# Kernel optimization log

Hardware: AMD Instinct MI355X
Metric: run time of the kernel (lower is better)

## Reference

```python
import math
import jax, jax.numpy as jnp
import numpy as np

N_HEADS = 32
ALIBI_BIAS_MAX = 8


def _alibi_slopes(n_heads, alibi_bias_max=8):
    _n = 2 ** math.ceil(math.log2(n_heads))
    m = jnp.arange(1, _n + 1, dtype=jnp.float32) * (alibi_bias_max / _n)
    slopes = 1.0 / jnp.power(2.0, m)
    if _n != n_heads:
        slopes = jnp.concatenate([slopes[1::2], slopes[::2]])[:n_heads]
    return slopes  # [H]


def setup_inputs() -> dict:
    key = jax.random.key(0)
    k1, k2, k3 = jax.random.split(key, 3)
    B, S, D = 1, 2048, 4096
    x = jax.random.normal(k1, (B, S, D), dtype=jnp.float32)
    w_qkv = jax.random.normal(k2, (3 * D, D), dtype=jnp.float32) * 0.02
    b_qkv = jnp.zeros((3 * D,), dtype=jnp.float32)
    w_out = jax.random.normal(k3, (D, D), dtype=jnp.float32) * 0.02
    b_out = jnp.zeros((D,), dtype=jnp.float32)
    return {"x": x, "w_qkv": w_qkv, "b_qkv": b_qkv, "w_out": w_out, "b_out": b_out}


def reference(x, w_qkv, b_qkv, w_out, b_out):
    B, S, D = x.shape
    H = N_HEADS
    hd = D // H
    # fused QKV projection (weights stored [Out, In], out_first=True)
    qkv = jnp.einsum("bsd,od->bso", x, w_qkv) + b_qkv  # [B,S,3D]
    q, k, v = jnp.split(qkv, 3, axis=-1)
    q = q.reshape(B, S, H, hd)
    k = k.reshape(B, S, H, hd)
    v = v.reshape(B, S, H, hd)
    scale = 1.0 / math.sqrt(hd)
    scores = jnp.einsum("bqhd,bkhd->bhqk", q, k) * scale  # [B,H,S,S]
    # ALiBi bias: slopes[h] * arange(1-KSeqLen, 1), broadcast over query pos
    slopes = _alibi_slopes(H, ALIBI_BIAS_MAX)  # [H]
    positions = jnp.arange(1 - S, 1, dtype=jnp.float32)  # [S] key positions
    alibi = slopes[:, None] * positions[None, :]  # [H, S_k]
    scores = scores + alibi[None, :, None, :]
    # causal mask
    causal = jnp.arange(S)[:, None] >= jnp.arange(S)[None, :]  # [Sq, Sk]
    scores = jnp.where(causal[None, None, :, :], scores, jnp.float32(-1e9))
    attn = jax.nn.softmax(scores, axis=-1)
    out = jnp.einsum("bhqk,bkhd->bqhd", attn, v).reshape(B, S, D)
    return jnp.einsum("bsd,od->bso", out, w_out) + b_out
```

## Files before the change

kernel.cpp:

```cpp
#include <hip/hip_runtime.h>
#include <hip/hip_bf16.h>

typedef __bf16 bf16;
typedef __attribute__((ext_vector_type(8))) __bf16 bf16x8;
typedef __attribute__((ext_vector_type(4))) float f32x4;

#define GLOAD_LDS16(g, l)                                                        \
    __builtin_amdgcn_global_load_lds(                                            \
        (const __attribute__((address_space(1))) void*)(g),                      \
        (__attribute__((address_space(3))) void*)(l), 16, 0, 0)

#define WAITV(n) asm volatile("s_waitcnt vmcnt(" #n ")" ::: "memory")
#define BAR()    __builtin_amdgcn_s_barrier()
#define SCHEDB() __builtin_amdgcn_sched_barrier(0)

__global__ __launch_bounds__(256) void cvt_f32_bf16(
    const float* __restrict__ src, bf16* __restrict__ dst, int n16)
{
    int idx = blockIdx.x * 256 + threadIdx.x;
    const int stride = gridDim.x * 256;
    for (int i = idx; i < n16; i += stride) {
        const float* p = src + (size_t)i * 16;
        f32x4 a = *(const f32x4*)p;
        f32x4 b = *(const f32x4*)(p + 4);
        f32x4 c = *(const f32x4*)(p + 8);
        f32x4 d = *(const f32x4*)(p + 12);
        bf16x8 h0, h1;
#pragma unroll
        for (int j = 0; j < 4; ++j) {
            h0[j] = (bf16)a[j]; h0[4 + j] = (bf16)b[j];
            h1[j] = (bf16)c[j]; h1[4 + j] = (bf16)d[j];
        }
        bf16* q = dst + (size_t)i * 16;
        *(bf16x8*)q = h0;
        *(bf16x8*)(q + 8) = h1;
    }
}

template <int OUT_BF16>
__global__ __launch_bounds__(512, 2) void gemm_sp(
    const bf16* __restrict__ A, const bf16* __restrict__ B,
    const float* __restrict__ bias, void* __restrict__ Cout,
    int K, int ldc, int nbx)
{
    constexpr int ASZ = 128 * 64;
    constexpr int BUF = ASZ + 256 * 64;
    __shared__ bf16 lds[3 * BUF];

    int bx, by;
    if ((nbx & 15) == 0) {
        const int r = (int)blockIdx.x & 255;
        const int slot = r >> 3;
        bx = ((int)blockIdx.x >> 8) * 16 + (r & 7) * 2 + (slot >> 4);
        by = slot & 15;
    } else {
        const int cpx = gridDim.x >> 3;
        const int swz = ((int)blockIdx.x & 7) * cpx + ((int)blockIdx.x >> 3);
        bx = swz % nbx; by = swz / nbx;
    }
    const int brow = by * 128, bcol = bx * 256;

    const int tid  = threadIdx.x;
    const int wv   = tid >> 6, lane = tid & 63;
    const int lo   = lane & 15, hi = lane >> 4;
    const int wrp  = wv >> 2, wcp = wv & 3;

    const int srow = lane >> 3;
    const int scol = ((lane & 7) ^ (lane >> 3)) * 8;

    f32x4 acc[4][4];
#pragma unroll
    for (int m = 0; m < 4; ++m)
#pragma unroll
        for (int n = 0; n < 4; ++n)
            acc[m][n] = (f32x4){0.f, 0.f, 0.f, 0.f};

    auto STAGE = [&](int t) {
        const int k0 = t * 64;
        bf16* lb = &lds[(t % 3) * BUF];
#pragma unroll
        for (int j = 0; j < 2; ++j) {
            const int c = wv * 2 + j;
            GLOAD_LDS16(A + (size_t)(brow + c * 8 + srow) * K + k0 + scol, lb + c * 512);
        }
#pragma unroll
        for (int j = 0; j < 4; ++j) {
            const int c = wv * 4 + j;
            GLOAD_LDS16(B + (size_t)(bcol + c * 8 + srow) * K + k0 + scol, lb + ASZ + c * 512);
        }
    };

    const int nt = K / 64;

    STAGE(0); STAGE(1);
    WAITV(6); BAR(); SCHEDB();

    for (int t = 0; t < nt; ++t) {
        const bf16* lb = &lds[(t % 3) * BUF];

        bf16x8 af[4][2], bfr[4][2];
#pragma unroll
        for (int m = 0; m < 4; ++m) {
            const int ru = wrp * 64 + m * 16 + lo;
#pragma unroll
            for (int kk = 0; kk < 2; ++kk)
                af[m][kk] = *(const bf16x8*)&lb[ru * 64 + (((kk * 4 + hi) ^ (lo & 7)) * 8)];
        }
#pragma unroll
        for (int n = 0; n < 4; ++n) {
            const int rb = wcp * 64 + n * 16 + lo;
#pragma unroll
            for (int kk = 0; kk < 2; ++kk)
                bfr[n][kk] = *(const bf16x8*)&lb[ASZ + rb * 64 + (((kk * 4 + hi) ^ (lo & 7)) * 8)];
        }

        if (t + 2 < nt) STAGE(t + 2);

        __builtin_amdgcn_s_setprio(1);
#pragma unroll
        for (int m = 0; m < 4; ++m)
#pragma unroll
            for (int n = 0; n < 4; ++n)
#pragma unroll
                for (int kk = 0; kk < 2; ++kk)
                    acc[m][n] = __builtin_amdgcn_mfma_f32_16x16x32_bf16(af[m][kk], bfr[n][kk], acc[m][n], 0, 0, 0);
        __builtin_amdgcn_s_setprio(0);

        if (t + 2 < nt)      WAITV(6);
        else if (t + 1 < nt) WAITV(0);
        if (t + 1 < nt) { BAR(); SCHEDB(); }
    }

#pragma unroll
    for (int m = 0; m < 4; ++m) {
        const int row = brow + wrp * 64 + m * 16 + hi * 4;
#pragma unroll
        for (int n = 0; n < 4; ++n) {
            const int col = bcol + wcp * 64 + n * 16 + lo;
            const float bv = bias[col];
#pragma unroll
            for (int r = 0; r < 4; ++r) {
                const float v = acc[m][n][r] + bv;
                if (OUT_BF16)
                    ((bf16*)Cout)[(size_t)(row + r) * ldc + col] = (bf16)v;
                else
                    ((float*)Cout)[(size_t)(row + r) * ldc + col] = v;
            }
        }
    }
}

__global__ __launch_bounds__(512) void attn_mfma(
    const bf16* __restrict__ qkv, bf16* __restrict__ attn_out)
{
    const int S = 2048, QKV = 12288, D = 4096, HD = 128;
    const int bid = blockIdx.x;
    const int h   = bid & 31;
    const int qi  = 15 - (bid >> 5);
    const int q0  = qi * 128;
    const int tid = threadIdx.x;
    const int w    = tid >> 6, lane = tid & 63;
    const int lo   = lane & 15, hi = lane >> 4;
    const int qbase = q0 + w * 16;

    __shared__ bf16 Ks[64 * 128];
    __shared__ bf16 Vs[128 * 72];
    __shared__ bf16 Ps[8 * 16 * 72];

    const float scale = 0.08838834764831845f;
    const float slope = exp2f(-0.25f * (float)(h + 1));

    bf16x8 qfrag[4];
#pragma unroll
    for (int ds = 0; ds < 4; ++ds)
        qfrag[ds] = *(const bf16x8*)(qkv + (size_t)(qbase + lo) * QKV + h * HD + ds * 32 + hi * 8);

    f32x4 o[8];
#pragma unroll
    for (int dt = 0; dt < 8; ++dt) o[dt] = (f32x4){0.f, 0.f, 0.f, 0.f};
    float mrow[4] = {-1e30f, -1e30f, -1e30f, -1e30f};
    float lrow[4] = {0.f, 0.f, 0.f, 0.f};

    const int krow = tid >> 3;
    const int kch  = tid & 7;
    const int vp2  = tid & 63;
    const int voct = tid >> 6;

    const int ntile = (q0 + 128) / 64;
    for (int t = 0; t < ntile; ++t) {
        const int kv0 = t * 64;
        {
            const bf16* kp = qkv + (size_t)(kv0 + krow) * QKV + D + h * HD + kch * 16;
            bf16x8 k0 = *(const bf16x8*)kp;
            bf16x8 k1 = *(const bf16x8*)(kp + 8);
            const int kb  = krow * 128 + kch * 16;
            const int swzk = (krow & 7) << 3;
            *(bf16x8*)&Ks[kb ^ swzk]       = k0;
            *(bf16x8*)&Ks[(kb + 8) ^ swzk] = k1;
        }
        {
            const bf16* vp = qkv + (size_t)(kv0 + voct * 8) * QKV + 2 * D + h * HD + 2 * vp2;
            bf16x8 r0, r1;
#pragma unroll
            for (int j = 0; j < 8; ++j) {
                const unsigned u = *(const unsigned*)(vp + (size_t)j * QKV);
                unsigned short us0 = (unsigned short)(u & 0xffff);
                unsigned short us1 = (unsigned short)(u >> 16);
                r0[j] = *(const bf16*)&us0;
                r1[j] = *(const bf16*)&us1;
            }
            *(bf16x8*)&Vs[(2 * vp2) * 72 + voct * 8]     = r0;
            *(bf16x8*)&Vs[(2 * vp2 + 1) * 72 + voct * 8] = r1;
        }
        __syncthreads();

        if (kv0 <= qbase + 15) {
            f32x4 c[4];
#pragma unroll
            for (int j = 0; j < 4; ++j) c[j] = (f32x4){0.f, 0.f, 0.f, 0.f};
            __builtin_amdgcn_s_setprio(1);
#pragma unroll
            for (int ds = 0; ds < 4; ++ds) {
#pragma unroll
                for (int j = 0; j < 4; ++j) {
                    const int r = j * 16 + lo;
                    bf16x8 b = *(const bf16x8*)&Ks[(r * 128 + ds * 32 + hi * 8) ^ ((r & 7) << 3)];
                    c[j] = __builtin_amdgcn_mfma_f32_16x16x32_bf16(qfrag[ds], b, c[j], 0, 0, 0);
                }
            }
            __builtin_amdgcn_s_setprio(0);
#pragma unroll
            for (int r = 0; r < 4; ++r) {
                const int q = qbase + hi * 4 + r;
                float s[4];
#pragma unroll
                for (int j = 0; j < 4; ++j) {
                    const int ki = kv0 + j * 16 + lo;
                    s[j] = c[j][r] * scale + slope * (float)(ki - (S - 1));
                    if (ki > q) s[j] = -1e30f;
                }
                float tm = fmaxf(fmaxf(s[0], s[1]), fmaxf(s[2], s[3]));
                tm = fmaxf(tm, __shfl_xor(tm, 1));
                tm = fmaxf(tm, __shfl_xor(tm, 2));
                tm = fmaxf(tm, __shfl_xor(tm, 4));
                tm = fmaxf(tm, __shfl_xor(tm, 8));
                const float mnew = fmaxf(mrow[r], tm);
                const float cr = __expf(mrow[r] - mnew);
                float p[4], ps = 0.f;
#pragma unroll
                for (int j = 0; j < 4; ++j) { p[j] = __expf(s[j] - mnew); ps += p[j]; }
                ps += __shfl_xor(ps, 1);
                ps += __shfl_xor(ps, 2);
                ps += __shfl_xor(ps, 4);
                ps += __shfl_xor(ps, 8);
                lrow[r] = lrow[r] * cr + ps;
                mrow[r] = mnew;
#pragma unroll
                for (int dt = 0; dt < 8; ++dt) o[dt][r] *= cr;
#pragma unroll
                for (int j = 0; j < 4; ++j)
                    Ps[w * 1152 + (hi * 4 + r) * 72 + j * 16 + lo] = (bf16)p[j];
            }
            bf16x8 pa0 = *(const bf16x8*)&Ps[w * 1152 + lo * 72 + hi * 8];
            bf16x8 pa1 = *(const bf16x8*)&Ps[w * 1152 + lo * 72 + 32 + hi * 8];
            __builtin_amdgcn_s_setprio(1);
#pragma unroll
            for (int dt = 0; dt < 8; ++dt) {
                bf16x8 bv0 = *(const bf16x8*)&Vs[(dt * 16 + lo) * 72 + hi * 8];
                bf16x8 bv1 = *(const bf16x8*)&Vs[(dt * 16 + lo) * 72 + 32 + hi * 8];
                o[dt] = __builtin_amdgcn_mfma_f32_16x16x32_bf16(pa0, bv0, o[dt], 0, 0, 0);
                o[dt] = __builtin_amdgcn_mfma_f32_16x16x32_bf16(pa1, bv1, o[dt], 0, 0, 0);
            }
            __builtin_amdgcn_s_setprio(0);
        }
        __syncthreads();
    }

#pragma unroll
    for (int r = 0; r < 4; ++r) {
        const float inv = 1.0f / lrow[r];
        const int q = qbase + hi * 4 + r;
        bf16* op = attn_out + (size_t)q * D + h * HD;
#pragma unroll
        for (int dt = 0; dt < 8; ++dt)
            op[dt * 16 + lo] = (bf16)(o[dt][r] * inv);
    }
}

extern "C" void kernel_launch(void* const* d_in, const int* in_sizes, int n_in,
                              void* d_out, int out_size, void* d_ws, size_t ws_size,
                              hipStream_t stream) {
    const int S = 2048, D = 4096, QKV = 12288;
    const int NH = 6144;
    const float* x     = (const float*)d_in[0];
    const float* w_qkv = (const float*)d_in[1];
    const float* b_qkv = (const float*)d_in[2];
    const float* w_out = (const float*)d_in[3];
    const float* b_out = (const float*)d_in[4];
    float* out = (float*)d_out;

    char* ws = (char*)d_ws;
    const size_t need_full = (size_t)S * D * 2 + (size_t)QKV * D * 2 + (size_t)S * QKV * 2;

    if (ws_size >= need_full) {
        bf16* xb    = (bf16*)ws;
        bf16* attnb = xb;
        bf16* wqb   = (bf16*)(ws + (size_t)S * D * 2);
        bf16* wob   = wqb;
        bf16* qkvb  = (bf16*)(ws + (size_t)S * D * 2 + (size_t)QKV * D * 2);

        cvt_f32_bf16<<<2048, 256, 0, stream>>>(x, xb, S * D / 16);
        cvt_f32_bf16<<<4096, 256, 0, stream>>>(w_qkv, wqb, QKV * D / 16);
        gemm_sp<1><<<(QKV / 256) * (S / 128), 512, 0, stream>>>(xb, wqb, b_qkv, qkvb, D, QKV, QKV / 256);
        attn_mfma<<<512, 512, 0, stream>>>(qkvb, attnb);
        cvt_f32_bf16<<<2048, 256, 0, stream>>>(w_out, wob, D * D / 16);
        gemm_sp<0><<<(D / 256) * (S / 128), 512, 0, stream>>>(attnb, wob, b_out, out, D, D, D / 256);
    } else {
        bf16* xb    = (bf16*)ws;
        bf16* attnb = xb;
        bf16* wb    = (bf16*)(ws + (size_t)S * D * 2);
        bf16* wob   = wb;
        bf16* qkvb  = (bf16*)(ws + (size_t)S * D * 2 + (size_t)NH * D * 2);

        cvt_f32_bf16<<<2048, 256, 0, stream>>>(x, xb, S * D / 16);
        cvt_f32_bf16<<<2048, 256, 0, stream>>>(w_qkv, wb, NH * D / 16);
        gemm_sp<1><<<(NH / 256) * (S / 128), 512, 0, stream>>>(xb, wb, b_qkv, qkvb, D, QKV, NH / 256);
        cvt_f32_bf16<<<2048, 256, 0, stream>>>(w_qkv + (size_t)NH * D, wb, NH * D / 16);
        gemm_sp<1><<<(NH / 256) * (S / 128), 512, 0, stream>>>(xb, wb, b_qkv + NH, qkvb + NH, D, QKV, NH / 256);
        attn_mfma<<<512, 512, 0, stream>>>(qkvb, attnb);
        cvt_f32_bf16<<<2048, 256, 0, stream>>>(w_out, wob, D * D / 16);
        gemm_sp<0><<<(D / 256) * (S / 128), 512, 0, stream>>>(attnb, wob, b_out, out, D, D, D / 256);
    }
}
```

Baseline: 435.0 us.

## Add 256x256-tile ping-pong GEMM with interleaved staging for QKV projection

Adds a new gemm_8p kernel that computes a 256x256 output tile per 512-thread block (each wave holds 8x4 accumulators) with a double-buffered LDS layout. Each K-step is split into four quarter-MFMA phases, and global->LDS staging for the next step is interleaved between them. Barriers and setprio calls are placed to get ping-pong overlap across waves. The QKV projection now uses this kernel with half as many blocks, which raises arithmetic intensity per block; the cost is more register pressure, many barriers, and fewer blocks in the grid (384) for the occupancy target.

New measurement: 465.6 us. 7.0% more time.

```diff
diff --git a/kernel.cpp b/kernel.cpp
--- a/kernel.cpp
+++ b/kernel.cpp
@@ -11,6 +11,7 @@
         (__attribute__((address_space(3))) void*)(l), 16, 0, 0)
 
 #define WAITV(n) asm volatile("s_waitcnt vmcnt(" #n ")" ::: "memory")
+#define LGKM0()  asm volatile("s_waitcnt lgkmcnt(0)" ::: "memory")
 #define BAR()    __builtin_amdgcn_s_barrier()
 #define SCHEDB() __builtin_amdgcn_sched_barrier(0)
 
@@ -38,6 +39,153 @@
 }
 
 template <int OUT_BF16>
+__global__ __launch_bounds__(512, 2) void gemm_8p(
+    const bf16* __restrict__ A, const bf16* __restrict__ B,
+    const float* __restrict__ bias, void* __restrict__ Cout,
+    int K, int ldc, int nbx)
+{
+    __shared__ bf16 lds[2 * 4 * 8192];
+
+    const int cpx = gridDim.x >> 3;
+    const int swz = ((int)blockIdx.x & 7) * cpx + ((int)blockIdx.x >> 3);
+    const int bx = swz % nbx, by = swz / nbx;
+    const int brow = by * 256, bcol = bx * 256;
+
+    const int tid  = threadIdx.x;
+    const int wv   = tid >> 6, lane = tid & 63;
+    const int lo   = lane & 15, hi = lane >> 4;
+    const int wrp  = wv >> 2, wcp = wv & 3;
+
+    const int srow = lane >> 3;
+    const int scol = ((lane & 7) ^ (lane >> 3)) * 8;
+
+    f32x4 acc[8][4];
+#pragma unroll
+    for (int m = 0; m < 8; ++m)
+#pragma unroll
+        for (int n = 0; n < 4; ++n)
+            acc[m][n] = (f32x4){0.f, 0.f, 0.f, 0.f};
+
+    auto STAGEA = [&](int t, int half) {
+        bf16* lb = &lds[(t & 1) * 32768 + half * 8192];
+        const bf16* gb = A + (size_t)(brow + half * 128) * K + t * 64;
+#pragma unroll
+        for (int j = 0; j < 2; ++j) {
+            const int c = wv * 2 + j;
+            GLOAD_LDS16(gb + (size_t)(c * 8 + srow) * K + scol, lb + c * 512);
+        }
+    };
+    auto STAGEB = [&](int t, int half) {
+        bf16* lb = &lds[(t & 1) * 32768 + (2 + half) * 8192];
+        const bf16* gb = B + (size_t)(bcol + half * 128) * K + t * 64;
+#pragma unroll
+        for (int j = 0; j < 2; ++j) {
+            const int c = wv * 2 + j;
+            GLOAD_LDS16(gb + (size_t)(c * 8 + srow) * K + scol, lb + c * 512);
+        }
+    };
+
+    bf16x8 af[4][2], bf0[2][2], bf1[2][2];
+    auto LDA = [&](int b, int mh) {
+        const bf16* base = &lds[b * 32768 + wrp * 8192];
+#pragma unroll
+        for (int m = 0; m < 4; ++m)
+#pragma unroll
+            for (int kk = 0; kk < 2; ++kk)
+                af[m][kk] = *(const bf16x8*)&base[(mh * 64 + m * 16 + lo) * 64 + (((kk * 4 + hi) ^ (lo & 7)) * 8)];
+    };
+    auto LDB = [&](int b, int nh, bf16x8 (&bfr)[2][2]) {
+        const bf16* base = &lds[b * 32768 + (2 + (wcp >> 1)) * 8192];
+#pragma unroll
+        for (int n = 0; n < 2; ++n)
+#pragma unroll
+            for (int kk = 0; kk < 2; ++kk)
+                bfr[n][kk] = *(const bf16x8*)&base[((wcp & 1) * 64 + nh * 32 + n * 16 + lo) * 64 + (((kk * 4 + hi) ^ (lo & 7)) * 8)];
+    };
+
+#define MM(mh, nh, BF)                                                                     \
+    do {                                                                                   \
+        __builtin_amdgcn_s_setprio(1);                                                     \
+        _Pragma("unroll")                                                                  \
+        for (int m = 0; m < 4; ++m)                                                        \
+            _Pragma("unroll")                                                              \
+            for (int n = 0; n < 2; ++n)                                                    \
+                _Pragma("unroll")                                                          \
+                for (int kk = 0; kk < 2; ++kk)                                             \
+                    acc[(mh) * 4 + m][(nh) * 2 + n] = __builtin_amdgcn_mfma_f32_16x16x32_bf16( \
+                        af[m][kk], BF[n][kk], acc[(mh) * 4 + m][(nh) * 2 + n], 0, 0, 0);   \
+        __builtin_amdgcn_s_setprio(0);                                                     \
+    } while (0)
+
+    const int nt = K / 64, niter = nt / 2;
+
+    STAGEA(0, 0); STAGEA(0, 1); STAGEB(0, 0); STAGEB(0, 1);
+    STAGEA(1, 0); STAGEA(1, 1); STAGEB(1, 0); STAGEB(1, 1);
+    WAITV(8); BAR(); SCHEDB();
+
+    for (int it = 0; it < niter; ++it) {
+        const int t0 = 2 * it;
+        const bool nl = (it + 1 < niter);
+
+        LDA(0, 0); LDB(0, 0, bf0);
+        BAR(); LGKM0(); SCHEDB();
+        MM(0, 0, bf0);
+        BAR();
+        LDB(0, 1, bf1);
+        BAR(); LGKM0(); SCHEDB();
+        MM(0, 1, bf1);
+        BAR();
+        LDA(0, 1);
+        if (nl) { STAGEB(t0 + 2, 0); STAGEB(t0 + 2, 1); }
+        BAR(); LGKM0(); SCHEDB();
+        MM(1, 1, bf1);
+        BAR();
+        if (nl) { STAGEA(t0 + 2, 0); STAGEA(t0 + 2, 1); }
+        BAR(); SCHEDB();
+        MM(1, 0, bf0);
+        if (nl) WAITV(8); else WAITV(0);
+        BAR(); SCHEDB();
+
+        LDA(1, 0); LDB(1, 0, bf0);
+        BAR(); LGKM0(); SCHEDB();
+        MM(0, 0, bf0);
+        BAR();
+        LDB(1, 1, bf1);
+        BAR(); LGKM0(); SCHEDB();
+        MM(0, 1, bf1);
+        BAR();
+        LDA(1, 1);
+        if (nl) { STAGEB(t0 + 3, 0); STAGEB(t0 + 3, 1); }
+        BAR(); LGKM0(); SCHEDB();
+        MM(1, 1, bf1);
+        BAR();
+        if (nl) { STAGEA(t0 + 3, 0); STAGEA(t0 + 3, 1); }
+        BAR(); SCHEDB();
+        MM(1, 0, bf0);
+        if (nl) { WAITV(8); BAR(); SCHEDB(); }
+    }
+#undef MM
+
+#pragma unroll
+    for (int mi = 0; mi < 8; ++mi) {
+        const int row = brow + wrp * 128 + mi * 16 + hi * 4;
+#pragma unroll
+        for (int ni = 0; ni < 4; ++ni) {
+            const int col = bcol + wcp * 64 + ni * 16 + lo;
+            const float bv = bias[col];
+#pragma unroll
+            for (int r = 0; r < 4; ++r) {
+                const float v = acc[mi][ni][r] + bv;
+                if (OUT_BF16)
+                    ((bf16*)Cout)[(size_t)(row + r) * ldc + col] = (bf16)v;
+                else
+                    ((float*)Cout)[(size_t)(row + r) * ldc + col] = v;
+            }
+        }
+    }
+}
+
+template <int OUT_BF16>
 __global__ __launch_bounds__(512, 2) void gemm_sp(
     const bf16* __restrict__ A, const bf16* __restrict__ B,
     const float* __restrict__ bias, void* __restrict__ Cout,
@@ -91,13 +239,11 @@
     };
 
     const int nt = K / 64;
-
     STAGE(0); STAGE(1);
     WAITV(6); BAR(); SCHEDB();
 
     for (int t = 0; t < nt; ++t) {
         const bf16* lb = &lds[(t % 3) * BUF];
-
         bf16x8 af[4][2], bfr[4][2];
 #pragma unroll
         for (int m = 0; m < 4; ++m) {
@@ -311,7 +457,7 @@
 
         cvt_f32_bf16<<<2048, 256, 0, stream>>>(x, xb, S * D / 16);
         cvt_f32_bf16<<<4096, 256, 0, stream>>>(w_qkv, wqb, QKV * D / 16);
-        gemm_sp<1><<<(QKV / 256) * (S / 128), 512, 0, stream>>>(xb, wqb, b_qkv, qkvb, D, QKV, QKV / 256);
+        gemm_8p<1><<<(QKV / 256) * (S / 256), 512, 0, stream>>>(xb, wqb, b_qkv, qkvb, D, QKV, QKV / 256);
         attn_mfma<<<512, 512, 0, stream>>>(qkvb, attnb);
         cvt_f32_bf16<<<2048, 256, 0, stream>>>(w_out, wob, D * D / 16);
         gemm_sp<0><<<(D / 256) * (S / 128), 512, 0, stream>>>(attnb, wob, b_out, out, D, D, D / 256);
@@ -324,9 +470,9 @@
 
         cvt_f32_bf16<<<2048, 256, 0, stream>>>(x, xb, S * D / 16);
         cvt_f32_bf16<<<2048, 256, 0, stream>>>(w_qkv, wb, NH * D / 16);
-        gemm_sp<1><<<(NH / 256) * (S / 128), 512, 0, stream>>>(xb, wb, b_qkv, qkvb, D, QKV, NH / 256);
+        gemm_8p<1><<<(NH / 256) * (S / 256), 512, 0, stream>>>(xb, wb, b_qkv, qkvb, D, QKV, NH / 256);
         cvt_f32_bf16<<<2048, 256, 0, stream>>>(w_qkv + (size_t)NH * D, wb, NH * D / 16);
-        gemm_sp<1><<<(NH / 256) * (S / 128), 512, 0, stream>>>(xb, wb, b_qkv + NH, qkvb + NH, D, QKV, NH / 256);
+        gemm_8p<1><<<(NH / 256) * (S / 256), 512, 0, stream>>>(xb, wb, b_qkv + NH, qkvb + NH, D, QKV, NH / 256);
         attn_mfma<<<512, 512, 0, stream>>>(qkvb, attnb);
         cvt_f32_bf16<<<2048, 256, 0, stream>>>(w_out, wob, D * D / 16);
         gemm_sp<0><<<(D / 256) * (S / 128), 512, 0, stream>>>(attnb, wob, b_out, out, D, D, D / 256);
```

## Give each attention wave two 16-row query groups and halve the block size

Applied to the files above, without the earlier changes.

The attention kernel now runs 4 waves of 256 threads per block instead of 8 waves of 512. Each wave handles 32 query rows as two 16-row groups, so every K fragment read from LDS feeds two QK MFMAs and every V fragment feeds two PV MFMAs. K and V tile loading is redistributed so each thread loads twice as much. This cuts LDS reads per MFMA, but it doubles the accumulator registers per wave and makes the causal skip coarser, which may hurt occupancy and load balance.

Result: slower. 476.2 us (+9.5%).

```diff
diff --git a/kernel.cpp b/kernel.cpp
--- a/kernel.cpp
+++ b/kernel.cpp
@@ -91,13 +91,11 @@
     };
 
     const int nt = K / 64;
-
     STAGE(0); STAGE(1);
     WAITV(6); BAR(); SCHEDB();
 
     for (int t = 0; t < nt; ++t) {
         const bf16* lb = &lds[(t % 3) * BUF];
-
         bf16x8 af[4][2], bfr[4][2];
 #pragma unroll
         for (int m = 0; m < 4; ++m) {
@@ -150,7 +148,7 @@
     }
 }
 
-__global__ __launch_bounds__(512) void attn_mfma(
+__global__ __launch_bounds__(256) void attn_mfma(
     const bf16* __restrict__ qkv, bf16* __restrict__ attn_out)
 {
     const int S = 2048, QKV = 12288, D = 4096, HD = 128;
@@ -161,63 +159,76 @@
     const int tid = threadIdx.x;
     const int w    = tid >> 6, lane = tid & 63;
     const int lo   = lane & 15, hi = lane >> 4;
-    const int qbase = q0 + w * 16;
+    const int qbase = q0 + w * 32;
 
     __shared__ bf16 Ks[64 * 128];
     __shared__ bf16 Vs[128 * 72];
-    __shared__ bf16 Ps[8 * 16 * 72];
+    __shared__ bf16 Ps[4 * 32 * 72];
 
     const float scale = 0.08838834764831845f;
     const float slope = exp2f(-0.25f * (float)(h + 1));
 
-    bf16x8 qfrag[4];
-#pragma unroll
-    for (int ds = 0; ds < 4; ++ds)
-        qfrag[ds] = *(const bf16x8*)(qkv + (size_t)(qbase + lo) * QKV + h * HD + ds * 32 + hi * 8);
-
-    f32x4 o[8];
-#pragma unroll
-    for (int dt = 0; dt < 8; ++dt) o[dt] = (f32x4){0.f, 0.f, 0.f, 0.f};
-    float mrow[4] = {-1e30f, -1e30f, -1e30f, -1e30f};
-    float lrow[4] = {0.f, 0.f, 0.f, 0.f};
-
-    const int krow = tid >> 3;
-    const int kch  = tid & 7;
+    bf16x8 qfrag[2][4];
+#pragma unroll
+    for (int qg = 0; qg < 2; ++qg)
+#pragma unroll
+        for (int ds = 0; ds < 4; ++ds)
+            qfrag[qg][ds] = *(const bf16x8*)(qkv + (size_t)(qbase + qg * 16 + lo) * QKV + h * HD + ds * 32 + hi * 8);
+
+    f32x4 o[2][8];
+#pragma unroll
+    for (int qg = 0; qg < 2; ++qg)
+#pragma unroll
+        for (int dt = 0; dt < 8; ++dt) o[qg][dt] = (f32x4){0.f, 0.f, 0.f, 0.f};
+    float mrow[2][4], lrow[2][4];
+#pragma unroll
+    for (int qg = 0; qg < 2; ++qg)
+#pragma unroll
+        for (int r = 0; r < 4; ++r) { mrow[qg][r] = -1e30f; lrow[qg][r] = 0.f; }
+
+    const int krow = tid >> 2;
+    const int kch  = tid & 3;
     const int vp2  = tid & 63;
-    const int voct = tid >> 6;
+    const int vgrp = tid >> 6;
 
     const int ntile = (q0 + 128) / 64;
     for (int t = 0; t < ntile; ++t) {
         const int kv0 = t * 64;
         {
-            const bf16* kp = qkv + (size_t)(kv0 + krow) * QKV + D + h * HD + kch * 16;
-            bf16x8 k0 = *(const bf16x8*)kp;
-            bf16x8 k1 = *(const bf16x8*)(kp + 8);
-            const int kb  = krow * 128 + kch * 16;
+            const bf16* kp = qkv + (size_t)(kv0 + krow) * QKV + D + h * HD + kch * 32;
+            const int kb  = krow * 128 + kch * 32;
             const int swzk = (krow & 7) << 3;
-            *(bf16x8*)&Ks[kb ^ swzk]       = k0;
-            *(bf16x8*)&Ks[(kb + 8) ^ swzk] = k1;
+#pragma unroll
+            for (int j = 0; j < 4; ++j) {
+                bf16x8 kv8 = *(const bf16x8*)(kp + j * 8);
+                *(bf16x8*)&Ks[(kb + j * 8) ^ swzk] = kv8;
+            }
         }
         {
-            const bf16* vp = qkv + (size_t)(kv0 + voct * 8) * QKV + 2 * D + h * HD + 2 * vp2;
-            bf16x8 r0, r1;
+            const bf16* vp = qkv + (size_t)(kv0 + vgrp * 16) * QKV + 2 * D + h * HD + 2 * vp2;
+            bf16x8 r0a, r0b, r1a, r1b;
 #pragma unroll
             for (int j = 0; j < 8; ++j) {
-                const unsigned u = *(const unsigned*)(vp + (size_t)j * QKV);
-                unsigned short us0 = (unsigned short)(u & 0xffff);
-                unsigned short us1 = (unsigned short)(u >> 16);
-                r0[j] = *(const bf16*)&us0;
-                r1[j] = *(const bf16*)&us1;
-            }
-            *(bf16x8*)&Vs[(2 * vp2) * 72 + voct * 8]     = r0;
-            *(bf16x8*)&Vs[(2 * vp2 + 1) * 72 + voct * 8] = r1;
+                unsigned u = *(const unsigned*)(vp + (size_t)j * QKV);
+                unsigned v = *(const unsigned*)(vp + (size_t)(8 + j) * QKV);
+                unsigned short u0 = (unsigned short)(u & 0xffff), u1 = (unsigned short)(u >> 16);
+                unsigned short v0 = (unsigned short)(v & 0xffff), v1 = (unsigned short)(v >> 16);
+                r0a[j] = *(const bf16*)&u0; r1a[j] = *(const bf16*)&u1;
+                r0b[j] = *(const bf16*)&v0; r1b[j] = *(const bf16*)&v1;
+            }
+            *(bf16x8*)&Vs[(2 * vp2) * 72 + vgrp * 16]         = r0a;
+            *(bf16x8*)&Vs[(2 * vp2) * 72 + vgrp * 16 + 8]     = r0b;
+            *(bf16x8*)&Vs[(2 * vp2 + 1) * 72 + vgrp * 16]     = r1a;
+            *(bf16x8*)&Vs[(2 * vp2 + 1) * 72 + vgrp * 16 + 8] = r1b;
         }
         __syncthreads();
 
-        if (kv0 <= qbase + 15) {
-            f32x4 c[4];
-#pragma unroll
-            for (int j = 0; j < 4; ++j) c[j] = (f32x4){0.f, 0.f, 0.f, 0.f};
+        if (kv0 <= qbase + 31) {
+            f32x4 c[2][4];
+#pragma unroll
+            for (int qg = 0; qg < 2; ++qg)
+#pragma unroll
+                for (int j = 0; j < 4; ++j) c[qg][j] = (f32x4){0.f, 0.f, 0.f, 0.f};
             __builtin_amdgcn_s_setprio(1);
 #pragma unroll
             for (int ds = 0; ds < 4; ++ds) {
@@ -225,51 +236,62 @@
                 for (int j = 0; j < 4; ++j) {
                     const int r = j * 16 + lo;
                     bf16x8 b = *(const bf16x8*)&Ks[(r * 128 + ds * 32 + hi * 8) ^ ((r & 7) << 3)];
-                    c[j] = __builtin_amdgcn_mfma_f32_16x16x32_bf16(qfrag[ds], b, c[j], 0, 0, 0);
+                    c[0][j] = __builtin_amdgcn_mfma_f32_16x16x32_bf16(qfrag[0][ds], b, c[0][j], 0, 0, 0);
+                    c[1][j] = __builtin_amdgcn_mfma_f32_16x16x32_bf16(qfrag[1][ds], b, c[1][j], 0, 0, 0);
                 }
             }
             __builtin_amdgcn_s_setprio(0);
 #pragma unroll
-            for (int r = 0; r < 4; ++r) {
-                const int q = qbase + hi * 4 + r;
-                float s[4];
-#pragma unroll
-                for (int j = 0; j < 4; ++j) {
-                    const int ki = kv0 + j * 16 + lo;
-                    s[j] = c[j][r] * scale + slope * (float)(ki - (S - 1));
-                    if (ki > q) s[j] = -1e30f;
+            for (int qg = 0; qg < 2; ++qg) {
+#pragma unroll
+                for (int r = 0; r < 4; ++r) {
+                    const int q = qbase + qg * 16 + hi * 4 + r;
+                    float s[4];
+#pragma unroll
+                    for (int j = 0; j < 4; ++j) {
+                        const int ki = kv0 + j * 16 + lo;
+                        s[j] = c[qg][j][r] * scale + slope * (float)(ki - (S - 1));
+                        if (ki > q) s[j] = -1e30f;
+                    }
+                    float tm = fmaxf(fmaxf(s[0], s[1]), fmaxf(s[2], s[3]));
+                    tm = fmaxf(tm, __shfl_xor(tm, 1));
+                    tm = fmaxf(tm, __shfl_xor(tm, 2));
+                    tm = fmaxf(tm, __shfl_xor(tm, 4));
+                    tm = fmaxf(tm, __shfl_xor(tm, 8));
+                    const float mnew = fmaxf(mrow[qg][r], tm);
+                    const float cr = __expf(mrow[qg][r] - mnew);
+                    float p[4], ps = 0.f;
+#pragma unroll
+                    for (int j = 0; j < 4; ++j) { p[j] = __expf(s[j] - mnew); ps += p[j]; }
+                    ps += __shfl_xor(ps, 1);
+                    ps += __shfl_xor(ps, 2);
+                    ps += __shfl_xor(ps, 4);
+                    ps += __shfl_xor(ps, 8);
+                    lrow[qg][r] = lrow[qg][r] * cr + ps;
+                    mrow[qg][r] = mnew;
+#pragma unroll
+                    for (int dt = 0; dt < 8; ++dt) o[qg][dt][r] *= cr;
+#pragma unroll
+                    for (int j = 0; j < 4; ++j)
+                        Ps[w * 2304 + (qg * 16 + hi * 4 + r) * 72 + j * 16 + lo] = (bf16)p[j];
                 }
-                float tm = fmaxf(fmaxf(s[0], s[1]), fmaxf(s[2], s[3]));
-                tm = fmaxf(tm, __shfl_xor(tm, 1));
-                tm = fmaxf(tm, __shfl_xor(tm, 2));
-                tm = fmaxf(tm, __shfl_xor(tm, 4));
-                tm = fmaxf(tm, __shfl_xor(tm, 8));
-                const float mnew = fmaxf(mrow[r], tm);
-                const float cr = __expf(mrow[r] - mnew);
-                float p[4], ps = 0.f;
-#pragma unroll
-                for (int j = 0; j < 4; ++j) { p[j] = __expf(s[j] - mnew); ps += p[j]; }
-                ps += __shfl_xor(ps, 1);
-                ps += __shfl_xor(ps, 2);
-                ps += __shfl_xor(ps, 4);
-                ps += __shfl_xor(ps, 8);
-                lrow[r] = lrow[r] * cr + ps;
-                mrow[r] = mnew;
-#pragma unroll
-                for (int dt = 0; dt < 8; ++dt) o[dt][r] *= cr;
-#pragma unroll
-                for (int j = 0; j < 4; ++j)
-                    Ps[w * 1152 + (hi * 4 + r) * 72 + j * 16 + lo] = (bf16)p[j];
-            }
-            bf16x8 pa0 = *(const bf16x8*)&Ps[w * 1152 + lo * 72 + hi * 8];
-            bf16x8 pa1 = *(const bf16x8*)&Ps[w * 1152 + lo * 72 + 32 + hi * 8];
+            }
+            bf16x8 pa0[2], pa1[2];
+#pragma unroll
+            for (int qg = 0; qg < 2; ++qg) {
+                pa0[qg] = *(const bf16x8*)&Ps[w * 2304 + (qg * 16 + lo) * 72 + hi * 8];
+                pa1[qg] = *(const bf16x8*)&Ps[w * 2304 + (qg * 16 + lo) * 72 + 32 + hi * 8];
+            }
             __builtin_amdgcn_s_setprio(1);
 #pragma unroll
             for (int dt = 0; dt < 8; ++dt) {
                 bf16x8 bv0 = *(const bf16x8*)&Vs[(dt * 16 + lo) * 72 + hi * 8];
                 bf16x8 bv1 = *(const bf16x8*)&Vs[(dt * 16 + lo) * 72 + 32 + hi * 8];
-                o[dt] = __builtin_amdgcn_mfma_f32_16x16x32_bf16(pa0, bv0, o[dt], 0, 0, 0);
-                o[dt] = __builtin_amdgcn_mfma_f32_16x16x32_bf16(pa1, bv1, o[dt], 0, 0, 0);
+#pragma unroll
+                for (int qg = 0; qg < 2; ++qg) {
+                    o[qg][dt] = __builtin_amdgcn_mfma_f32_16x16x32_bf16(pa0[qg], bv0, o[qg][dt], 0, 0, 0);
+                    o[qg][dt] = __builtin_amdgcn_mfma_f32_16x16x32_bf16(pa1[qg], bv1, o[qg][dt], 0, 0, 0);
+                }
             }
             __builtin_amdgcn_s_setprio(0);
         }
@@ -277,14 +299,16 @@
     }
 
 #pragma unroll
-    for (int r = 0; r < 4; ++r) {
-        const float inv = 1.0f / lrow[r];
-        const int q = qbase + hi * 4 + r;
-        bf16* op = attn_out + (size_t)q * D + h * HD;
-#pragma unroll
-        for (int dt = 0; dt < 8; ++dt)
-            op[dt * 16 + lo] = (bf16)(o[dt][r] * inv);
-    }
+    for (int qg = 0; qg < 2; ++qg)
+#pragma unroll
+        for (int r = 0; r < 4; ++r) {
+            const float inv = 1.0f / lrow[qg][r];
+            const int q = qbase + qg * 16 + hi * 4 + r;
+            bf16* op = attn_out + (size_t)q * D + h * HD;
+#pragma unroll
+            for (int dt = 0; dt < 8; ++dt)
+                op[dt * 16 + lo] = (bf16)(o[qg][dt][r] * inv);
+        }
 }
 
 extern "C" void kernel_launch(void* const* d_in, const int* in_sizes, int n_in,
@@ -312,7 +336,7 @@
         cvt_f32_bf16<<<2048, 256, 0, stream>>>(x, xb, S * D / 16);
         cvt_f32_bf16<<<4096, 256, 0, stream>>>(w_qkv, wqb, QKV * D / 16);
         gemm_sp<1><<<(QKV / 256) * (S / 128), 512, 0, stream>>>(xb, wqb, b_qkv, qkvb, D, QKV, QKV / 256);
-        attn_mfma<<<512, 512, 0, stream>>>(qkvb, attnb);
+        attn_mfma<<<512, 256, 0, stream>>>(qkvb, attnb);
         cvt_f32_bf16<<<2048, 256, 0, stream>>>(w_out, wob, D * D / 16);
         gemm_sp<0><<<(D / 256) * (S / 128), 512, 0, stream>>>(attnb, wob, b_out, out, D, D, D / 256);
     } else {
@@ -327,7 +351,7 @@
         gemm_sp<1><<<(NH / 256) * (S / 128), 512, 0, stream>>>(xb, wb, b_qkv, qkvb, D, QKV, NH / 256);
         cvt_f32_bf16<<<2048, 256, 0, stream>>>(w_qkv + (size_t)NH * D, wb, NH * D / 16);
         gemm_sp<1><<<(NH / 256) * (S / 128), 512, 0, stream>>>(xb, wb, b_qkv + NH, qkvb + NH, D, QKV, NH / 256);
-        attn_mfma<<<512, 512, 0, stream>>>(qkvb, attnb);
+        attn_mfma<<<512, 256, 0, stream>>>(qkvb, attnb);
         cvt_f32_bf16<<<2048, 256, 0, stream>>>(w_out, wob, D * D / 16);
         gemm_sp<0><<<(D / 256) * (S / 128), 512, 0, stream>>>(attnb, wob, b_out, out, D, D, D / 256);
     }
```
